# Optimization experiments

Hardware: AMD Instinct MI355X
Metric: run time of the kernel (lower is better)

The kernel has to match this reference:

```python
import math
import jax, jax.numpy as jnp
import numpy as np
from jax.scipy.special import xlogy

B, N, INP, E = 128, 16, 1024, 512
MU, CLF, PLCY = 512, 512, 512
M = N - 1          # merges (full tree)
T = N + M          # total tree tokens
L = N + M - 1      # logits matrix side
NOISE_STD, MASK_VAL = 0.01, -9e20
SFTMX_EPS, STD_EPS = 1e-20, 1e-20


def _mlp3(x, w1, b1, w2, b2, w3, b3):
    h = jax.nn.relu(x @ w1 + b1)
    h = jax.nn.relu(h @ w2 + b2)
    return h @ w3 + b3


def _lin(key, fi, fo):
    lim = math.sqrt(6.0 / (fi + fo))  # xavier uniform
    return (jax.random.uniform(key, (fi, fo), minval=-lim, maxval=lim, dtype=jnp.float32),
            jnp.full((fo,), 0.001, dtype=jnp.float32))


def setup_inputs():
    key = jax.random.key(0)
    ks = jax.random.split(key, 16)
    inp = {"x": jax.random.normal(ks[0], (B, N, INP), dtype=jnp.float32)}
    inp["lift_w"], inp["lift_b"] = _lin(ks[1], INP, E)
    inp["unlift_w"], inp["unlift_b"] = _lin(ks[2], E, INP)
    inp["enc_w1"], inp["enc_b1"] = _lin(ks[3], 2 * E, MU)
    inp["enc_w2"], inp["enc_b2"] = _lin(ks[4], MU, MU)
    inp["enc_w3"], inp["enc_b3"] = _lin(ks[5], MU, E)
    inp["dec_w1"], inp["dec_b1"] = _lin(ks[6], E, MU)
    inp["dec_w2"], inp["dec_b2"] = _lin(ks[7], MU, MU)
    inp["dec_w3"], inp["dec_b3"] = _lin(ks[8], MU, 2 * E)
    inp["clf_w1"], inp["clf_b1"] = _lin(ks[9], E, CLF)
    inp["clf_w2"], inp["clf_b2"] = _lin(ks[10], CLF, CLF)
    inp["clf_w3"], inp["clf_b3"] = _lin(ks[11], CLF, 2)
    inp["pol_w1"], inp["pol_b1"] = _lin(ks[12], 2 * E, PLCY)
    inp["pol_w2"], inp["pol_b2"] = _lin(ks[13], PLCY, PLCY)
    inp["pol_w3"], inp["pol_b3"] = _lin(ks[14], PLCY, 1)
    return inp


def _forward(x, lift_w, lift_b, unlift_w, unlift_b,
             enc_w1, enc_b1, enc_w2, enc_b2, enc_w3, enc_b3,
             dec_w1, dec_b1, dec_w2, dec_b2, dec_w3, dec_b3,
             clf_w1, clf_b1, clf_w2, clf_b2, clf_w3, clf_b3,
             pol_w1, pol_b1, pol_w2, pol_b2, pol_w3, pol_b3):
    sg = jax.lax.stop_gradient
    enc = lambda z: _mlp3(z, enc_w1, enc_b1, enc_w2, enc_b2, enc_w3, enc_b3)
    dec = lambda z: _mlp3(z, dec_w1, dec_b1, dec_w2, dec_b2, dec_w3, dec_b3)
    clf = lambda z: _mlp3(z, clf_w1, clf_b1, clf_w2, clf_b2, clf_w3, clf_b3)
    pol = lambda z: _mlp3(z, pol_w1, pol_b1, pol_w2, pol_b2, pol_w3, pol_b3)
    base = jax.random.key(42)
    b_idx = jnp.arange(B)

    # lift + noise
    u = x @ lift_w + lift_b
    u = u + NOISE_STD * jax.random.normal(jax.random.fold_in(base, 7), u.shape, u.dtype)

    logits_mtx = jnp.full((B, L, L), MASK_VAL, dtype=jnp.float32)
    # iter 0: score all ordered pairs (i,j), i != j, among input tokens (vectorized)
    ii, jj = np.where(~np.eye(N, dtype=bool))                 # P = N*(N-1) static pairs
    pair_x = jnp.concatenate([u[:, ii], u[:, jj]], axis=-1)   # [B,P,2E]
    logits_mtx = logits_mtx.at[:, ii, jj].set(pol(sg(pair_x))[..., 0])

    active = jnp.tile(jnp.arange(N, dtype=jnp.int32), (B, 1))
    step_losses = jnp.zeros(B, dtype=jnp.float32)
    entropies = jnp.zeros(B, dtype=jnp.float32)
    actions, log_probs, rewards = [], [], []

    for it in range(M):
        A = active.shape[1]  # = N - it (active-token count at entry)
        if it > 0:
            nt = N + it - 1                      # newest merged token (last in active)
            act = active[:, :-1]                 # [B, A-1] older active tokens
            u_act = u[b_idx[:, None], act]       # [B, A-1, E]
            u_nt = jnp.broadcast_to(u[:, nt][:, None, :], u_act.shape)
            lg_f = pol(sg(jnp.concatenate([u_nt, u_act], -1)))[..., 0]
            lg_b = pol(sg(jnp.concatenate([u_act, u_nt], -1)))[..., 0]
            logits_mtx = logits_mtx.at[b_idx[:, None], nt, act].set(lg_f)
            logits_mtx = logits_mtx.at[b_idx[:, None], act, nt].set(lg_b)

        flat = logits_mtx.reshape(B, L * L)      # temp == 1 for learned policy
        p = jax.nn.softmax(flat, axis=1)
        P2 = L * L
        p_adj = (p + SFTMX_EPS) / (1.0 + P2 * SFTMX_EPS)
        val_norm = SFTMX_EPS / (1.0 + P2 * SFTMX_EPS)
        opt_norm = A * (A - 1)
        nopt = P2 - opt_norm
        entrop = -(jnp.sum(xlogy(p_adj, p_adj), axis=1)
                   - nopt * (val_norm * math.log(val_norm))) / math.log(opt_norm)
        entropies = entropies + entrop

        # multinomial sample over flattened (masked) logits matrix
        sflat = jax.random.categorical(jax.random.fold_in(base, 100 + it), flat)
        s0, s1 = sflat // L, sflat % L
        sample = jnp.stack([s0, s1], axis=1)     # [B,2]
        actions.append(sample)
        log_probs.append(jnp.log(p[b_idx, sflat]))

        # mask out rows/cols of the merged tokens
        logits_mtx = logits_mtx.at[b_idx[:, None], sample, :].set(MASK_VAL)
        logits_mtx = logits_mtx.at[b_idx[:, None], :, sample].set(MASK_VAL)

        # remove the two sampled tokens from the active set (order-preserving)
        keep = (active != s0[:, None].astype(active.dtype)) & (active != s1[:, None].astype(active.dtype))
        order = jnp.argsort((~keep).astype(jnp.int32), axis=1, stable=True)
        active = jnp.take_along_axis(active, order[:, :A - 2], axis=1)

        pair = jnp.concatenate([u[b_idx, s0], u[b_idx, s1]], axis=1)  # [B,2E]
        true_s = sg(pair)
        pred_s = dec(enc(true_s))
        osl = jnp.sum((pred_s - true_s) ** 2, axis=1) / (2 * E)
        step_losses = step_losses + osl
        rewards.append(-sg(osl))

        # merge: encode pair (grad flows into u here) + noise, append to tree
        mg = enc(pair)
        mg = mg + NOISE_STD * jax.random.normal(jax.random.fold_in(base, 1000 + it), mg.shape, mg.dtype)
        u = jnp.concatenate([u, mg[:, None, :]], axis=1)
        active = jnp.concatenate([active, jnp.full((B, 1), N + it, dtype=active.dtype)], axis=1)

    actions = jnp.stack(actions, axis=1)    # [B,M,2]
    log_probs = jnp.stack(log_probs, axis=1)
    rewards = jnp.stack(rewards, axis=1)

    # top-down decode
    d = jnp.zeros_like(u)
    d = d.at[b_idx[:, None], active].set(u[b_idx[:, None], active])  # seed remaining active (root)
    clf_rows = []
    for it in range(M):
        tok = T - 1 - it
        mgd = d[:, tok]
        unmg = dec(mgd).reshape(B, 2, E)
        d = d.at[b_idx[:, None], actions[:, M - 1 - it]].set(unmg)
        clf_rows.append(clf(sg(mgd)))
    clf_pred = jnp.concatenate(
        [jnp.stack(clf_rows, axis=1), clf(sg(d[:, :N]))[:, ::-1, :]], axis=1)  # [B,M+N,2]
    clf_lbl = jnp.tile(jnp.concatenate(
        [jnp.ones(M, dtype=jnp.int32), jnp.zeros(N, dtype=jnp.int32)]), (B, 1))

    step_losses = step_losses / M
    entropies = entropies / M
    mvg = rewards.reshape(-1)  # B*M <= mvg_adv_sz, so moving buffer == current rewards
    rew_n = (rewards - mvg.mean()) / (jnp.std(mvg, ddof=1) + STD_EPS)
    reinf = jnp.sum(log_probs * rew_n, axis=1)
    recon = d[:, :N] @ unlift_w + unlift_b
    return recon, u, d, step_losses, entropies, clf_pred, clf_lbl, reinf


def reference(x, lift_w, lift_b, unlift_w, unlift_b,
              enc_w1, enc_b1, enc_w2, enc_b2, enc_w3, enc_b3,
              dec_w1, dec_b1, dec_w2, dec_b2, dec_w3, dec_b3,
              clf_w1, clf_b1, clf_w2, clf_b2, clf_w3, clf_b3,
              pol_w1, pol_b1, pol_w2, pol_b2, pol_w3, pol_b3):
    return _forward(x, lift_w, lift_b, unlift_w, unlift_b,
                    enc_w1, enc_b1, enc_w2, enc_b2, enc_w3, enc_b3,
                    dec_w1, dec_b1, dec_w2, dec_b2, dec_w3, dec_b3,
                    clf_w1, clf_b1, clf_w2, clf_b2, clf_w3, clf_b3,
                    pol_w1, pol_b1, pol_w2, pol_b2, pol_w3, pol_b3)
```

## Files before the change

kernel.cpp:

```cpp
#include <hip/hip_runtime.h>
#include <cstdint>
#include <cmath>

#define MASKV -9.0e20f

__host__ __device__ inline void tf2x32(uint32_t k0, uint32_t k1, uint32_t& x0, uint32_t& x1){
  uint32_t ks2 = k0 ^ k1 ^ 0x1BD11BDAu;
  x0 += k0; x1 += k1;
#define TFR(r) { x0 += x1; x1 = (x1<<(r))|(x1>>(32-(r))); x1 ^= x0; }
  TFR(13) TFR(15) TFR(26) TFR(6)
  x0 += k1;  x1 += ks2 + 1u;
  TFR(17) TFR(29) TFR(16) TFR(24)
  x0 += ks2; x1 += k0 + 2u;
  TFR(13) TFR(15) TFR(26) TFR(6)
  x0 += k0;  x1 += k1 + 3u;
  TFR(17) TFR(29) TFR(16) TFR(24)
  x0 += k1;  x1 += ks2 + 4u;
  TFR(13) TFR(15) TFR(26) TFR(6)
  x0 += ks2; x1 += k0 + 5u;
#undef TFR
}

__device__ inline uint32_t rbits32(uint32_t k0, uint32_t k1, uint32_t idx){
  uint32_t x0 = 0u, x1 = idx;
  tf2x32(k0, k1, x0, x1);
  return x0 ^ x1;
}

__device__ inline float u01_from_bits(uint32_t bits){
  union { uint32_t u; float f; } c;
  c.u = (bits >> 9) | 0x3f800000u;
  return c.f - 1.0f;
}

__device__ inline float erfinv_f(float x){
  float w = -log1pf(-x*x);
  float p;
  if (w < 5.0f){
    w -= 2.5f;
    p = 2.81022636e-08f;
    p = fmaf(p, w, 3.43273939e-07f);
    p = fmaf(p, w, -3.5233877e-06f);
    p = fmaf(p, w, -4.39150654e-06f);
    p = fmaf(p, w, 0.00021858087f);
    p = fmaf(p, w, -0.00125372503f);
    p = fmaf(p, w, -0.00417768164f);
    p = fmaf(p, w, 0.246640727f);
    p = fmaf(p, w, 1.50140941f);
  } else {
    w = sqrtf(w) - 3.0f;
    p = -0.000200214257f;
    p = fmaf(p, w, 0.000100950558f);
    p = fmaf(p, w, 0.00134934322f);
    p = fmaf(p, w, -0.00367342844f);
    p = fmaf(p, w, 0.00573950773f);
    p = fmaf(p, w, -0.0076224613f);
    p = fmaf(p, w, 0.00943887047f);
    p = fmaf(p, w, 1.00167406f);
    p = fmaf(p, w, 2.83297682f);
  }
  return p * x;
}

__device__ inline float jax_normal(uint32_t k0, uint32_t k1, uint32_t idx){
  float f = u01_from_bits(rbits32(k0, k1, idx));
  float v = fmaf(f, 2.0f, -0.99999994f);
  v = fmaxf(v, -0.99999994f);
  return 1.41421356f * erfinv_f(v);
}

__device__ inline float jax_gumbel(uint32_t k0, uint32_t k1, uint32_t idx){
  float f = u01_from_bits(rbits32(k0, k1, idx));
  f = f + 1.17549435e-38f;
  f = fmaxf(f, 1.17549435e-38f);
  return -logf(-logf(f));
}

template<int ACT>
__global__ __launch_bounds__(256) void gemm_k(
    const float* __restrict__ A, int lda,
    const long* __restrict__ atab, int anblk,
    const float* __restrict__ W, const float* __restrict__ bias,
    float* __restrict__ C, int K, int N,
    long c_base, int c_rdiv, long c_ostride, long c_istride)
{
  __shared__ float As[16][64];
  __shared__ float Ws[16][64];
  int tid = threadIdx.x;
  int c0 = blockIdx.x * 64;
  int r0 = blockIdx.y * 64;
  int lr = tid >> 2;
  int lk = (tid & 3) << 2;
  int wk = tid >> 4;
  int wc = (tid & 15) << 2;
  int tx = tid & 15;
  int ty = tid >> 4;
  long aoff0 = 0, aoff1 = 0;
  if (atab){
    const long* t = atab + (long)(r0 + lr) * anblk;
    aoff0 = t[0];
    if (anblk == 2) aoff1 = t[1];
  } else {
    aoff0 = (long)(r0 + lr) * lda;
  }
  float acc[4][4];
#pragma unroll
  for (int i = 0; i < 4; i++)
#pragma unroll
    for (int j = 0; j < 4; j++) acc[i][j] = 0.f;

  for (int k0 = 0; k0 < K; k0 += 16){
    int ka = k0 + lk;
    long ab = (atab && anblk == 2 && ka >= 512) ? (aoff1 + (ka - 512)) : (aoff0 + ka);
    float4 av = *(const float4*)(A + ab);
    As[lk + 0][lr] = av.x;
    As[lk + 1][lr] = av.y;
    As[lk + 2][lr] = av.z;
    As[lk + 3][lr] = av.w;
    float4 wv = *(const float4*)(W + (long)(k0 + wk) * N + (c0 + wc));
    *(float4*)&Ws[wk][wc] = wv;
    __syncthreads();
#pragma unroll
    for (int kk = 0; kk < 16; kk++){
      float4 a4 = *(const float4*)&As[kk][ty << 2];
      float4 w4 = *(const float4*)&Ws[kk][tx << 2];
      float aa[4] = {a4.x, a4.y, a4.z, a4.w};
      float ww[4] = {w4.x, w4.y, w4.z, w4.w};
#pragma unroll
      for (int i = 0; i < 4; i++)
#pragma unroll
        for (int j = 0; j < 4; j++)
          acc[i][j] = fmaf(aa[i], ww[j], acc[i][j]);
    }
    __syncthreads();
  }
  float4 bv = *(const float4*)(bias + c0 + (tx << 2));
  float bb[4] = {bv.x, bv.y, bv.z, bv.w};
#pragma unroll
  for (int i = 0; i < 4; i++){
    int r = r0 + (ty << 2) + i;
    long off = c_base + (long)(r / c_rdiv) * c_ostride + (long)(r % c_rdiv) * c_istride
               + c0 + (tx << 2);
    float4 v;
    float o0 = acc[i][0] + bb[0], o1 = acc[i][1] + bb[1];
    float o2 = acc[i][2] + bb[2], o3 = acc[i][3] + bb[3];
    if (ACT){ o0 = fmaxf(o0, 0.f); o1 = fmaxf(o1, 0.f); o2 = fmaxf(o2, 0.f); o3 = fmaxf(o3, 0.f); }
    v.x = o0; v.y = o1; v.z = o2; v.w = o3;
    *(float4*)(C + off) = v;
  }
}

__global__ __launch_bounds__(256) void gemm128f_k(
    const float* __restrict__ Y,
    const long* __restrict__ atab,
    const float* __restrict__ b1,
    const float* __restrict__ W2, const float* __restrict__ b2,
    const float* __restrict__ w3,
    const int* __restrict__ scat, float* __restrict__ logits)
{
  __shared__ float As[16][132];
  __shared__ float Ws[16][132];
  int tid = threadIdx.x;
  int c0 = blockIdx.x * 128;
  int r0 = blockIdx.y * 128;
  int tx = tid & 15, ty = tid >> 4;
  int rA0 = tid >> 2;
  int rA1 = rA0 + 64;
  int kq = (tid & 3) << 2;
  long a00 = atab[(long)(r0 + rA0) * 2];
  long a01 = atab[(long)(r0 + rA0) * 2 + 1];
  long a10 = atab[(long)(r0 + rA1) * 2];
  long a11 = atab[(long)(r0 + rA1) * 2 + 1];
  int wk0 = tid >> 5, wc0 = (tid & 31) << 2;
  float acc[8][8];
#pragma unroll
  for (int i = 0; i < 8; i++)
#pragma unroll
    for (int j = 0; j < 8; j++) acc[i][j] = 0.f;

  for (int k0 = 0; k0 < 512; k0 += 16){
    int ka = k0 + kq;
    float4 p0 = *(const float4*)(Y + a00 + ka);
    float4 q0 = *(const float4*)(Y + a01 + ka);
    float4 p1 = *(const float4*)(Y + a10 + ka);
    float4 q1 = *(const float4*)(Y + a11 + ka);
    float4 bb = *(const float4*)(b1 + ka);
    As[kq + 0][rA0] = fmaxf(p0.x + q0.x + bb.x, 0.f);
    As[kq + 1][rA0] = fmaxf(p0.y + q0.y + bb.y, 0.f);
    As[kq + 2][rA0] = fmaxf(p0.z + q0.z + bb.z, 0.f);
    As[kq + 3][rA0] = fmaxf(p0.w + q0.w + bb.w, 0.f);
    As[kq + 0][rA1] = fmaxf(p1.x + q1.x + bb.x, 0.f);
    As[kq + 1][rA1] = fmaxf(p1.y + q1.y + bb.y, 0.f);
    As[kq + 2][rA1] = fmaxf(p1.z + q1.z + bb.z, 0.f);
    As[kq + 3][rA1] = fmaxf(p1.w + q1.w + bb.w, 0.f);
    *(float4*)&Ws[wk0][wc0]     = *(const float4*)(W2 + (long)(k0 + wk0) * 512 + (c0 + wc0));
    *(float4*)&Ws[wk0 + 8][wc0] = *(const float4*)(W2 + (long)(k0 + wk0 + 8) * 512 + (c0 + wc0));
    __syncthreads();
#pragma unroll
    for (int kk = 0; kk < 16; kk++){
      float a0[8], w0[8];
      *(float4*)&a0[0] = *(const float4*)&As[kk][ty << 2];
      *(float4*)&a0[4] = *(const float4*)&As[kk][(ty << 2) + 64];
      *(float4*)&w0[0] = *(const float4*)&Ws[kk][tx << 2];
      *(float4*)&w0[4] = *(const float4*)&Ws[kk][(tx << 2) + 64];
#pragma unroll
      for (int i = 0; i < 8; i++)
#pragma unroll
        for (int j = 0; j < 8; j++)
          acc[i][j] = fmaf(a0[i], w0[j], acc[i][j]);
    }
    __syncthreads();
  }
  float bb[8], w3v[8];
  *(float4*)&bb[0]  = *(const float4*)(b2 + c0 + (tx << 2));
  *(float4*)&bb[4]  = *(const float4*)(b2 + c0 + (tx << 2) + 64);
  *(float4*)&w3v[0] = *(const float4*)(w3 + c0 + (tx << 2));
  *(float4*)&w3v[4] = *(const float4*)(w3 + c0 + (tx << 2) + 64);
#pragma unroll
  for (int i = 0; i < 8; i++){
    float p = 0.f;
#pragma unroll
    for (int j = 0; j < 8; j++)
      p = fmaf(fmaxf(acc[i][j] + bb[j], 0.f), w3v[j], p);
    for (int m = 1; m < 16; m <<= 1) p += __shfl_xor(p, m);
    if (tx == 0){
      int rr = (i < 4) ? ((ty << 2) + i) : (64 + (ty << 2) + (i - 4));
      atomicAdd(logits + scat[r0 + rr], p);
    }
  }
}

__global__ __launch_bounds__(256) void gemm64f_k(
    const float* __restrict__ Y,
    const long* __restrict__ atab,
    const float* __restrict__ b1,
    const float* __restrict__ W2, const float* __restrict__ b2,
    const float* __restrict__ w3,
    const int* __restrict__ scat, float* __restrict__ logits)
{
  __shared__ float As[16][64];
  __shared__ float Ws[16][64];
  int tid = threadIdx.x;
  int c0 = blockIdx.x * 64;
  int r0 = blockIdx.y * 64;
  int lr = tid >> 2;
  int lk = (tid & 3) << 2;
  int wk = tid >> 4;
  int wc = (tid & 15) << 2;
  int tx = tid & 15;
  int ty = tid >> 4;
  long a0 = atab[(long)(r0 + lr) * 2];
  long a1 = atab[(long)(r0 + lr) * 2 + 1];
  float acc[4][4];
#pragma unroll
  for (int i = 0; i < 4; i++)
#pragma unroll
    for (int j = 0; j < 4; j++) acc[i][j] = 0.f;

  for (int k0 = 0; k0 < 512; k0 += 16){
    int ka = k0 + lk;
    float4 p = *(const float4*)(Y + a0 + ka);
    float4 q = *(const float4*)(Y + a1 + ka);
    float4 bb = *(const float4*)(b1 + ka);
    As[lk + 0][lr] = fmaxf(p.x + q.x + bb.x, 0.f);
    As[lk + 1][lr] = fmaxf(p.y + q.y + bb.y, 0.f);
    As[lk + 2][lr] = fmaxf(p.z + q.z + bb.z, 0.f);
    As[lk + 3][lr] = fmaxf(p.w + q.w + bb.w, 0.f);
    *(float4*)&Ws[wk][wc] = *(const float4*)(W2 + (long)(k0 + wk) * 512 + (c0 + wc));
    __syncthreads();
#pragma unroll
    for (int kk = 0; kk < 16; kk++){
      float4 a4 = *(const float4*)&As[kk][ty << 2];
      float4 w4 = *(const float4*)&Ws[kk][tx << 2];
      float aa[4] = {a4.x, a4.y, a4.z, a4.w};
      float ww[4] = {w4.x, w4.y, w4.z, w4.w};
#pragma unroll
      for (int i = 0; i < 4; i++)
#pragma unroll
        for (int j = 0; j < 4; j++)
          acc[i][j] = fmaf(aa[i], ww[j], acc[i][j]);
    }
    __syncthreads();
  }
  float bb4[4], w34[4];
  *(float4*)&bb4[0] = *(const float4*)(b2 + c0 + (tx << 2));
  *(float4*)&w34[0] = *(const float4*)(w3 + c0 + (tx << 2));
#pragma unroll
  for (int i = 0; i < 4; i++){
    float p = 0.f;
#pragma unroll
    for (int j = 0; j < 4; j++)
      p = fmaf(fmaxf(acc[i][j] + bb4[j], 0.f), w34[j], p);
    for (int m = 1; m < 16; m <<= 1) p += __shfl_xor(p, m);
    if (tx == 0){
      int r = r0 + (ty << 2) + i;
      atomicAdd(logits + scat[r], p);
    }
  }
}

__global__ __launch_bounds__(256) void rowdot2_k(
    const float* __restrict__ A, int lda,
    const float* __restrict__ W, const float* __restrict__ bias,
    int K, float* __restrict__ out, const int* __restrict__ scat)
{
  int wid = threadIdx.x >> 6, lane = threadIdx.x & 63;
  int r = blockIdx.x * 4 + wid;
  const float* a = A + (long)r * lda;
  float s0 = 0.f, s1 = 0.f;
  for (int k = lane; k < K; k += 64){
    float x = a[k];
    s0 = fmaf(x, W[k * 2], s0);
    s1 = fmaf(x, W[k * 2 + 1], s1);
  }
  for (int off = 32; off > 0; off >>= 1){
    s0 += __shfl_down(s0, off);
    s1 += __shfl_down(s1, off);
  }
  if (lane == 0){
    long o = scat[r];
    out[o] = s0 + bias[0];
    out[o + 1] = s1 + bias[1];
  }
}

__global__ __launch_bounds__(256) void pairmv_k(
    const float* __restrict__ u, const long* __restrict__ tab_pair,
    const float* __restrict__ W, const float* __restrict__ bias,
    float* __restrict__ dst)
{
  __shared__ float s[1024];
  int b = blockIdx.y, tid = threadIdx.x;
  int c = blockIdx.x * 256 + tid;
  long t0 = tab_pair[b * 2], t1 = tab_pair[b * 2 + 1];
  s[tid]       = u[t0 + tid];
  s[tid + 256] = u[t0 + tid + 256];
  s[tid + 512] = u[t1 + tid];
  s[tid + 768] = u[t1 + tid + 256];
  __syncthreads();
  float a0 = 0.f, a1 = 0.f, a2 = 0.f, a3 = 0.f;
#pragma unroll 8
  for (int k = 0; k < 1024; k += 4){
    a0 = fmaf(s[k],     W[(long)k * 512 + c],       a0);
    a1 = fmaf(s[k + 1], W[(long)(k + 1) * 512 + c], a1);
    a2 = fmaf(s[k + 2], W[(long)(k + 2) * 512 + c], a2);
    a3 = fmaf(s[k + 3], W[(long)(k + 3) * 512 + c], a3);
  }
  float v = ((a0 + a1) + (a2 + a3)) + bias[c];
  dst[(long)b * 512 + c] = fmaxf(v, 0.f);
}

__global__ __launch_bounds__(256) void mvrelu_k(
    const float* __restrict__ src, long sstride,
    const float* __restrict__ W, const float* __restrict__ bias,
    float* __restrict__ dst)
{
  __shared__ float s[512];
  int b = blockIdx.y, tid = threadIdx.x;
  int c = blockIdx.x * 256 + tid;
  const float* sr = src + (long)b * sstride;
  s[tid] = sr[tid];
  s[tid + 256] = sr[tid + 256];
  __syncthreads();
  float a0 = 0.f, a1 = 0.f, a2 = 0.f, a3 = 0.f;
#pragma unroll 8
// ... 101 lines not shown
    float d0 = p[k] - t0[k];       s = fmaf(d0, d0, s);
    float d1 = p[k + 512] - t1[k]; s = fmaf(d1, d1, s);
  }
  __shared__ float red[256];
  red[tid] = s; __syncthreads();
  for (int st = 128; st > 0; st >>= 1){ if (tid < st) red[tid] += red[tid + st]; __syncthreads(); }
  if (tid == 0){
    float osl = red[0] / 1024.0f;
    atomicAdd(sl + b, osl);
    rew[b * 15 + it] = -osl;
  }
}

__global__ __launch_bounds__(256) void init_k(float* __restrict__ lbl,
    float* __restrict__ logits, float* __restrict__ sl, float* __restrict__ ent,
    int* __restrict__ active, float* __restrict__ zb,
    float* __restrict__ W1cat, const float* __restrict__ pol_w1, const float* __restrict__ pol_b3,
    long* __restrict__ tab_init, int* __restrict__ scat_init, long* __restrict__ tab_tok16,
    long* __restrict__ tab_mgd, int* __restrict__ scat_clf, long clf_off)
{
  long i = (long)blockIdx.x * 256 + threadIdx.x;
  if (i < 524288L){
    int k = (int)(i >> 10), n = (int)(i & 1023);
    W1cat[i] = (n < 512) ? pol_w1[(long)k * 512 + n] : pol_w1[(long)(k + 512) * 512 + (n - 512)];
  }
  if (i < 115200L){
    int rem = (int)(i % 900);
    int rr = rem / 30, cc = rem % 30;
    logits[i] = (rr < 16 && cc < 16 && rr != cc) ? pol_b3[0] : MASKV;
  }
  if (i < 30720L){
    int r = (int)i;
    int pk = r >> 7, b = r & 127;
    int ii2 = pk / 15, jr = pk % 15;
    int jj2 = jr + (jr >= ii2 ? 1 : 0);
    tab_init[r * 2]     = ((long)(b * 31 + ii2)) * 1024;
    tab_init[r * 2 + 1] = ((long)(b * 31 + jj2)) * 1024 + 512;
    scat_init[r] = b * 900 + ii2 * 30 + jj2;
  }
  if (i < 3968L){
    lbl[i] = ((i % 31) < 15) ? 1.0f : 0.0f;
    int r = (int)i;
    if (r < 1920){
      scat_clf[r] = (int)(clf_off + (long)(r & 127) * 62 + (r >> 7) * 2);
    } else {
      int rr = r - 1920;
      scat_clf[r] = (int)(clf_off + (long)(rr >> 4) * 62 + 60 - ((rr & 15) << 1));
    }
  }
  if (i < 2048L){
    active[i] = (int)(i & 15);
    tab_tok16[i] = ((long)((i >> 4) * 31 + (i & 15))) * 512;
  }
  if (i < 1920L){
    int it = (int)(i >> 7), b = (int)(i & 127);
    tab_mgd[i] = ((long)(b * 31 + 30 - it)) * 512;
  }
  if (i < 1024L)  zb[i] = 0.f;
  if (i < 128L){ sl[i] = 0.f; ent[i] = 0.f; }
}

__global__ __launch_bounds__(256) void noise_u_k(float* __restrict__ u, uint32_t k0, uint32_t k1){
  uint32_t e = blockIdx.x * 256u + threadIdx.x;
  uint32_t b = e >> 13, rem = e & 8191u, n = rem >> 9, ee = rem & 511u;
  float nr = jax_normal(k0, k1, e);
  long off = ((long)(b * 31u + n)) * 512 + ee;
  u[off] += 0.01f * nr;
}

__global__ __launch_bounds__(256) void build_d_k(float* __restrict__ dmat, const float* __restrict__ u){
  int e = blockIdx.x * 256 + threadIdx.x;
  int b = e >> 9, ee = e & 511;
  long off = ((long)(b * 31 + 30)) * 512 + ee;
  dmat[off] = u[off];
}

__global__ __launch_bounds__(256) void sample_k(float* __restrict__ logits, int* __restrict__ active,
    int* __restrict__ actions, float* __restrict__ lp, float* __restrict__ ent,
    int it, int A, uint32_t k0, uint32_t k1, float log_opt,
    long* __restrict__ tab_loop, int* __restrict__ scat_loop, long* __restrict__ tab_pair,
    const float* __restrict__ pol_b3)
{
  int b = blockIdx.x, tid = threadIdx.x;
  float* Lg = logits + (long)b * 900;
  __shared__ float red[256];
  __shared__ int redi[256];
  __shared__ int ss0, ss1;

  float v = -3.4e38f;
  for (int j = tid; j < 900; j += 256) v = fmaxf(v, Lg[j]);
  red[tid] = v; __syncthreads();
  for (int s = 128; s > 0; s >>= 1){ if (tid < s) red[tid] = fmaxf(red[tid], red[tid + s]); __syncthreads(); }
  float m = red[0]; __syncthreads();

  float acc = 0.f;
  for (int j = tid; j < 900; j += 256) acc += expf(Lg[j] - m);
  red[tid] = acc; __syncthreads();
  for (int s = 128; s > 0; s >>= 1){ if (tid < s) red[tid] += red[tid + s]; __syncthreads(); }
  float ssum = red[0]; __syncthreads();

  float es = 0.f;
  for (int j = tid; j < 900; j += 256){
    float l = Lg[j];
    if (l > MASKV){
      float p = expf(l - m) / ssum;
      float pa = p + 1e-20f;
      es += pa * logf(pa);
    }
  }
  red[tid] = es; __syncthreads();
  for (int s = 128; s > 0; s >>= 1){ if (tid < s) red[tid] += red[tid + s]; __syncthreads(); }
  if (tid == 0) ent[b] += -(red[0]) / log_opt;
  __syncthreads();

  float bv = -3.4e38f; int bi = 0;
  for (int j = tid; j < 900; j += 256){
    float g = jax_gumbel(k0, k1, (uint32_t)(b * 900 + j));
    float val = Lg[j] + g;
    if (val > bv){ bv = val; bi = j; }
  }
  red[tid] = bv; redi[tid] = bi; __syncthreads();
  for (int s = 128; s > 0; s >>= 1){
    if (tid < s){
      float o = red[tid + s]; int oi = redi[tid + s];
      if (o > red[tid] || (o == red[tid] && oi < redi[tid])){ red[tid] = o; redi[tid] = oi; }
    }
    __syncthreads();
  }
  if (tid == 0){
    int sf = redi[0];
    int s0 = sf / 30, s1 = sf % 30;
    ss0 = s0; ss1 = s1;
    actions[(b * 15 + it) * 2] = s0;
    actions[(b * 15 + it) * 2 + 1] = s1;
    lp[b * 15 + it] = Lg[sf] - m - logf(ssum);
    tab_pair[b * 2]     = ((long)(b * 31 + s0)) * 512;
    tab_pair[b * 2 + 1] = ((long)(b * 31 + s1)) * 512;
  }
  __syncthreads();
  int s0 = ss0, s1 = ss1;
  if (tid < 30){
    Lg[s0 * 30 + tid] = MASKV;
    Lg[s1 * 30 + tid] = MASKV;
    Lg[tid * 30 + s0] = MASKV;
    Lg[tid * 30 + s1] = MASKV;
  }
  if (tid == 0){
    float b3v = pol_b3[0];
    int buf[16]; int c = 0;
    for (int k = 0; k < A; k++){
      int a = active[b * 16 + k];
      if (a != s0 && a != s1) buf[c++] = a;
    }
    int nt2 = 16 + it;
    buf[c++] = nt2;
    for (int k = 0; k < c; k++) active[b * 16 + k] = buf[k];
    int na2 = c - 1;
    for (int j = 0; j < na2; j++){
      int q = buf[j];
      int r1 = j * 128 + b;
      tab_loop[r1 * 2]     = ((long)(b * 31 + nt2)) * 1024;
      tab_loop[r1 * 2 + 1] = ((long)(b * 31 + q)) * 1024 + 512;
      int sc1 = b * 900 + nt2 * 30 + q;
      scat_loop[r1] = sc1;
      logits[sc1] = b3v;
      int r2 = (na2 + j) * 128 + b;
      tab_loop[r2 * 2]     = ((long)(b * 31 + q)) * 1024;
      tab_loop[r2 * 2 + 1] = ((long)(b * 31 + nt2)) * 1024 + 512;
      int sc2 = b * 900 + q * 30 + nt2;
      scat_loop[r2] = sc2;
      logits[sc2] = b3v;
    }
  }
}

__global__ __launch_bounds__(256) void finalize_k(const float* __restrict__ rew,
    const float* __restrict__ lp, const float* __restrict__ sl, const float* __restrict__ ent,
    float* __restrict__ out_sl, float* __restrict__ out_ent, float* __restrict__ out_reinf)
{
  __shared__ float red[256];
  int tid = threadIdx.x;
  float s = 0.f;
  for (int i = tid; i < 1920; i += 256) s += rew[i];
  red[tid] = s; __syncthreads();
  for (int st = 128; st > 0; st >>= 1){ if (tid < st) red[tid] += red[tid + st]; __syncthreads(); }
  float mean = red[0] / 1920.0f; __syncthreads();
  float v = 0.f;
  for (int i = tid; i < 1920; i += 256){ float x = rew[i] - mean; v = fmaf(x, x, v); }
  red[tid] = v; __syncthreads();
  for (int st = 128; st > 0; st >>= 1){ if (tid < st) red[tid] += red[tid + st]; __syncthreads(); }
  float denom = sqrtf(red[0] / 1919.0f) + 1e-20f;
  if (tid < 128){
    out_sl[tid] = sl[tid] / 15.0f;
    out_ent[tid] = ent[tid] / 15.0f;
    float r = 0.f;
    for (int k = 0; k < 15; k++){
      float rn = (rew[tid * 15 + k] - mean) / denom;
      r = fmaf(lp[tid * 15 + k], rn, r);
    }
    out_reinf[tid] = r;
  }
}

extern "C" void kernel_launch(void* const* d_in, const int* in_sizes, int n_in,
                              void* d_out, int out_size, void* d_ws, size_t ws_size,
                              hipStream_t stream)
{
  const float* x        = (const float*)d_in[0];
  const float* lift_w   = (const float*)d_in[1];
  const float* lift_b   = (const float*)d_in[2];
  const float* unlift_w = (const float*)d_in[3];
  const float* unlift_b = (const float*)d_in[4];
  const float* enc_w1   = (const float*)d_in[5];
  const float* enc_b1   = (const float*)d_in[6];
  const float* enc_w2   = (const float*)d_in[7];
  const float* enc_b2   = (const float*)d_in[8];
  const float* enc_w3   = (const float*)d_in[9];
  const float* enc_b3   = (const float*)d_in[10];
// ... 7 lines not shown
  const float* clf_b1   = (const float*)d_in[18];
  const float* clf_w2   = (const float*)d_in[19];
  const float* clf_b2   = (const float*)d_in[20];
  const float* clf_w3   = (const float*)d_in[21];
  const float* clf_b3   = (const float*)d_in[22];
  const float* pol_w1   = (const float*)d_in[23];
  const float* pol_b1   = (const float*)d_in[24];
  const float* pol_w2   = (const float*)d_in[25];
  const float* pol_b2   = (const float*)d_in[26];
  const float* pol_w3   = (const float*)d_in[27];
  const float* pol_b3   = (const float*)d_in[28];

  float* out = (float*)d_out;
  const long U_OFF     = 2097152;
  const long D_OFF     = 4128768;
  const long SL_OFF    = 6160384;
  const long ENT_OFF   = 6160512;
  const long CLF_OFF   = 6160640;
  const long LBL_OFF   = 6168576;
  const long REINF_OFF = 6172544;
  float* recon = out;
  float* u     = out + U_OFF;
  float* dmat  = out + D_OFF;

  char* wsb = (char*)d_ws;
  size_t wo = 0;
  auto alloc = [&](size_t bytes) -> void* {
    void* p = (void*)(wsb + wo);
    wo = (wo + bytes + 255) & ~(size_t)255;
    return p;
  };
  float* logits    = (float*)alloc(115200 * 4);
  float* Y         = (float*)alloc((size_t)3968 * 1024 * 4);
  float* h1clf     = Y;
  float* pbuf      = Y + 2031616;
  float* h2clf     = Y + 2031616;
  float* W1cat     = (float*)alloc((size_t)524288 * 4);
  float* zb        = (float*)alloc(1024 * 4);
  float* h1        = (float*)alloc((size_t)2048 * 512 * 4);
  float* h2        = (float*)alloc((size_t)2048 * 512 * 4);
  float* z_all     = (float*)alloc((size_t)15 * 65536 * 4);
  float* sl        = (float*)alloc(128 * 4);
  float* ent       = (float*)alloc(128 * 4);
  float* lp        = (float*)alloc(1920 * 4);
  float* rew       = (float*)alloc(1920 * 4);
  int*   active    = (int*)alloc(2048 * 4);
  int*   actions   = (int*)alloc(3840 * 4);
  long*  tab_init  = (long*)alloc((size_t)30720 * 2 * 8);
  int*   scat_init = (int*)alloc(30720 * 4);
  long*  tab_loop  = (long*)alloc((size_t)3584 * 2 * 8);
  int*   scat_loop = (int*)alloc(3584 * 4);
  long*  tab_pair  = (long*)alloc(256 * 8);
  long*  tab_mgd   = (long*)alloc(1920 * 8);
  long*  tab_tok16 = (long*)alloc(2048 * 8);
  int*   scat_clf  = (int*)alloc(3968 * 4);
  long*  tab_clf   = tab_mgd;
  (void)ws_size; (void)in_sizes; (void)n_in; (void)out_size;

  uint32_t k7a, k7b, ck0[15], ck1[15], mk0[15], mk1[15];
  { uint32_t a = 0, b = 7; tf2x32(0u, 42u, a, b); k7a = a; k7b = b; }
  for (int it = 0; it < 15; it++){
    { uint32_t a = 0, b = (uint32_t)(100 + it); tf2x32(0u, 42u, a, b); ck0[it] = a; ck1[it] = b; }
    { uint32_t a = 0, b = (uint32_t)(1000 + it); tf2x32(0u, 42u, a, b); mk0[it] = a; mk1[it] = b; }
  }

  auto gemm = [&](int act, const float* A, int lda, const long* atab, int anblk,
                  const float* W, const float* bs, float* C, int rows, int K, int Nn,
                  long cb, int crd, long cos, long cis){
    dim3 g(Nn / 64, rows / 64);
    if (act) gemm_k<1><<<g, 256, 0, stream>>>(A, lda, atab, anblk, W, bs, C, K, Nn, cb, crd, cos, cis);
    else     gemm_k<0><<<g, 256, 0, stream>>>(A, lda, atab, anblk, W, bs, C, K, Nn, cb, crd, cos, cis);
  };

  init_k<<<2048, 256, 0, stream>>>(out + LBL_OFF, logits, sl, ent, active, zb,
                                   W1cat, pol_w1, pol_b3, tab_init, scat_init, tab_tok16,
                                   tab_mgd, scat_clf, CLF_OFF);

  gemm(0, x, 1024, nullptr, 0, lift_w, lift_b, u, 2048, 1024, 512, 0, 16, 15872, 512);
  noise_u_k<<<4096, 256, 0, stream>>>(u, k7a, k7b);

  gemm(0, u, 0, tab_tok16, 1, W1cat, zb, Y, 2048, 512, 1024, 0, 16, 31744, 1024);

  { dim3 g(4, 240);
    gemm128f_k<<<g, 256, 0, stream>>>(Y, tab_init, pol_b1, pol_w2, pol_b2, pol_w3,
                                      scat_init, logits); }

  for (int it = 0; it < 15; it++){
    int A = 16 - it;
    if (it > 0){
      int rows = 256 * (15 - it);
      dim3 g(8, rows / 64);
      gemm64f_k<<<g, 256, 0, stream>>>(Y, tab_loop, pol_b1, pol_w2, pol_b2, pol_w3,
                                       scat_loop, logits);
    }
    float log_opt = (float)log((double)(A * (A - 1)));
    sample_k<<<128, 256, 0, stream>>>(logits, active, actions, lp, ent, it, A,
                                      ck0[it], ck1[it], log_opt,
                                      tab_loop, scat_loop, tab_pair, pol_b3);
    { dim3 g(2, 128);
      pairmv_k<<<g, 256, 0, stream>>>(u, tab_pair, enc_w1, enc_b1, h1); }
    { dim3 g(2, 128);
      mvrelu_k<<<g, 256, 0, stream>>>(h1, 512, enc_w2, enc_b2, h2); }
    { dim3 g(2, 128);
      lay3z_k<<<g, 256, 0, stream>>>(h2, enc_w3, enc_b3, z_all, u, it, mk0[it], mk1[it]); }
    if (it < 14){
      dim3 g(4, 128);
      yrow_k<<<g, 256, 0, stream>>>(u, W1cat, Y, it);
    }
  }

  gemm(1, z_all, 512, nullptr, 0, dec_w1, dec_b1, h1, 1920, 512, 512, 0, 1, 512, 0);
  gemm(1, h1, 512, nullptr, 0, dec_w2, dec_b2, h2, 1920, 512, 512, 0, 1, 512, 0);
  gemm(0, h2, 512, nullptr, 0, dec_w3, dec_b3, pbuf, 1920, 512, 1024, 0, 1, 1024, 0);
  oslb_k<<<1920, 256, 0, stream>>>(pbuf, u, actions, sl, rew);

  build_d_k<<<256, 256, 0, stream>>>(dmat, u);

  for (int it = 0; it < 15; it++){
    int tok = 30 - it;
    { dim3 g(2, 128);
      mvrelu_k<<<g, 256, 0, stream>>>(dmat + (long)tok * 512, 15872, dec_w1, dec_b1, h1); }
    { dim3 g(2, 128);
      mvrelu_k<<<g, 256, 0, stream>>>(h1, 512, dec_w2, dec_b2, h2); }
    { dim3 g(4, 128);
      rev3_k<<<g, 256, 0, stream>>>(h2, dec_w3, dec_b3, dmat, actions, it); }
  }

  gemm(1, dmat, 0, tab_clf, 1, clf_w1, clf_b1, h1clf, 3968, 512, 512, 0, 1, 512, 0);
  gemm(1, h1clf, 512, nullptr, 0, clf_w2, clf_b2, h2clf, 3968, 512, 512, 0, 1, 512, 0);
  rowdot2_k<<<992, 256, 0, stream>>>(h2clf, 512, clf_w3, clf_b3, 512, out, scat_clf);

  gemm(0, dmat, 0, tab_tok16, 1, unlift_w, unlift_b, recon, 2048, 512, 1024,
       0, 16, 16384, 1024);

  finalize_k<<<1, 256, 0, stream>>>(rew, lp, sl, ent,
                                    out + SL_OFF, out + ENT_OFF, out + REINF_OFF);
}
```

Measured before the change: 2.578 ms.

## Double-buffer shared tiles in GEMM kernels and use wave-shuffle reductions in sampling

The three SGEMM kernels now keep two shared-memory tile buffers and prefetch the next K-slice into registers while computing on the current one, so each iteration needs one barrier instead of two and global load latency overlaps the FMAs. The sampling kernel replaces tree reductions in shared memory with 64-lane shuffle reductions plus a small cross-wave step. It also computes entropy algebraically from a single pass (sum of e*d over S, minus log S), removing a reduction pass. The changes cost more shared memory and registers, which may lower occupancy, and the algebraic entropy can differ slightly in floating-point rounding from the original.

```diff
diff --git a/kernel.cpp b/kernel.cpp
--- a/kernel.cpp
+++ b/kernel.cpp
@@ -84,8 +84,8 @@
     float* __restrict__ C, int K, int N,
     long c_base, int c_rdiv, long c_ostride, long c_istride)
 {
-  __shared__ float As[16][64];
-  __shared__ float Ws[16][64];
+  __shared__ float As[2][16][64];
+  __shared__ float Ws[2][16][64];
   int tid = threadIdx.x;
   int c0 = blockIdx.x * 64;
   int r0 = blockIdx.y * 64;
@@ -109,21 +109,30 @@
 #pragma unroll
     for (int j = 0; j < 4; j++) acc[i][j] = 0.f;
 
+  {
+    float4 av = *(const float4*)(A + aoff0 + lk);
+    As[0][lk + 0][lr] = av.x;
+    As[0][lk + 1][lr] = av.y;
+    As[0][lk + 2][lr] = av.z;
+    As[0][lk + 3][lr] = av.w;
+    *(float4*)&Ws[0][wk][wc] = *(const float4*)(W + (long)wk * N + (c0 + wc));
+  }
+  __syncthreads();
+
+  int pb = 0;
   for (int k0 = 0; k0 < K; k0 += 16){
-    int ka = k0 + lk;
-    long ab = (atab && anblk == 2 && ka >= 512) ? (aoff1 + (ka - 512)) : (aoff0 + ka);
-    float4 av = *(const float4*)(A + ab);
-    As[lk + 0][lr] = av.x;
-    As[lk + 1][lr] = av.y;
-    As[lk + 2][lr] = av.z;
-    As[lk + 3][lr] = av.w;
-    float4 wv = *(const float4*)(W + (long)(k0 + wk) * N + (c0 + wc));
-    *(float4*)&Ws[wk][wc] = wv;
-    __syncthreads();
+    int nk = k0 + 16;
+    float4 av, wv;
+    if (nk < K){
+      int ka = nk + lk;
+      long ab = (atab && anblk == 2 && ka >= 512) ? (aoff1 + (ka - 512)) : (aoff0 + ka);
+      av = *(const float4*)(A + ab);
+      wv = *(const float4*)(W + (long)(nk + wk) * N + (c0 + wc));
+    }
 #pragma unroll
     for (int kk = 0; kk < 16; kk++){
-      float4 a4 = *(const float4*)&As[kk][ty << 2];
-      float4 w4 = *(const float4*)&Ws[kk][tx << 2];
+      float4 a4 = *(const float4*)&As[pb][kk][ty << 2];
+      float4 w4 = *(const float4*)&Ws[pb][kk][tx << 2];
       float aa[4] = {a4.x, a4.y, a4.z, a4.w};
       float ww[4] = {w4.x, w4.y, w4.z, w4.w};
 #pragma unroll
@@ -132,7 +141,16 @@
         for (int j = 0; j < 4; j++)
           acc[i][j] = fmaf(aa[i], ww[j], acc[i][j]);
     }
+    if (nk < K){
+      int nb = pb ^ 1;
+      As[nb][lk + 0][lr] = av.x;
+      As[nb][lk + 1][lr] = av.y;
+      As[nb][lk + 2][lr] = av.z;
+      As[nb][lk + 3][lr] = av.w;
+      *(float4*)&Ws[nb][wk][wc] = wv;
+    }
     __syncthreads();
+    pb ^= 1;
   }
   float4 bv = *(const float4*)(bias + c0 + (tx << 2));
   float bb[4] = {bv.x, bv.y, bv.z, bv.w};
@@ -158,8 +176,8 @@
     const float* __restrict__ w3,
     const int* __restrict__ scat, float* __restrict__ logits)
 {
-  __shared__ float As[16][132];
-  __shared__ float Ws[16][132];
+  __shared__ float As[2][16][132];
+  __shared__ float Ws[2][16][132];
   int tid = threadIdx.x;
   int c0 = blockIdx.x * 128;
   int r0 = blockIdx.y * 128;
@@ -178,38 +196,67 @@
 #pragma unroll
     for (int j = 0; j < 8; j++) acc[i][j] = 0.f;
 
+  {
+    float4 p0 = *(const float4*)(Y + a00 + kq);
+    float4 q0 = *(const float4*)(Y + a01 + kq);
+    float4 p1 = *(const float4*)(Y + a10 + kq);
+    float4 q1 = *(const float4*)(Y + a11 + kq);
+    float4 bb = *(const float4*)(b1 + kq);
+    As[0][kq + 0][rA0] = fmaxf(p0.x + q0.x + bb.x, 0.f);
+    As[0][kq + 1][rA0] = fmaxf(p0.y + q0.y + bb.y, 0.f);
+    As[0][kq + 2][rA0] = fmaxf(p0.z + q0.z + bb.z, 0.f);
+    As[0][kq + 3][rA0] = fmaxf(p0.w + q0.w + bb.w, 0.f);
+    As[0][kq + 0][rA1] = fmaxf(p1.x + q1.x + bb.x, 0.f);
+    As[0][kq + 1][rA1] = fmaxf(p1.y + q1.y + bb.y, 0.f);
+    As[0][kq + 2][rA1] = fmaxf(p1.z + q1.z + bb.z, 0.f);
+    As[0][kq + 3][rA1] = fmaxf(p1.w + q1.w + bb.w, 0.f);
+    *(float4*)&Ws[0][wk0][wc0]     = *(const float4*)(W2 + (long)wk0 * 512 + (c0 + wc0));
+    *(float4*)&Ws[0][wk0 + 8][wc0] = *(const float4*)(W2 + (long)(wk0 + 8) * 512 + (c0 + wc0));
+  }
+  __syncthreads();
+
+  int pb = 0;
   for (int k0 = 0; k0 < 512; k0 += 16){
-    int ka = k0 + kq;
-    float4 p0 = *(const float4*)(Y + a00 + ka);
-    float4 q0 = *(const float4*)(Y + a01 + ka);
-    float4 p1 = *(const float4*)(Y + a10 + ka);
-    float4 q1 = *(const float4*)(Y + a11 + ka);
-    float4 bb = *(const float4*)(b1 + ka);
-    As[kq + 0][rA0] = fmaxf(p0.x + q0.x + bb.x, 0.f);
-    As[kq + 1][rA0] = fmaxf(p0.y + q0.y + bb.y, 0.f);
-    As[kq + 2][rA0] = fmaxf(p0.z + q0.z + bb.z, 0.f);
-    As[kq + 3][rA0] = fmaxf(p0.w + q0.w + bb.w, 0.f);
-    As[kq + 0][rA1] = fmaxf(p1.x + q1.x + bb.x, 0.f);
-    As[kq + 1][rA1] = fmaxf(p1.y + q1.y + bb.y, 0.f);
-    As[kq + 2][rA1] = fmaxf(p1.z + q1.z + bb.z, 0.f);
-    As[kq + 3][rA1] = fmaxf(p1.w + q1.w + bb.w, 0.f);
-    *(float4*)&Ws[wk0][wc0]     = *(const float4*)(W2 + (long)(k0 + wk0) * 512 + (c0 + wc0));
-    *(float4*)&Ws[wk0 + 8][wc0] = *(const float4*)(W2 + (long)(k0 + wk0 + 8) * 512 + (c0 + wc0));
-    __syncthreads();
+    int nk = k0 + 16;
+    float4 p0, q0, p1, q1, bb, w0v, w1v;
+    if (nk < 512){
+      int ka = nk + kq;
+      p0 = *(const float4*)(Y + a00 + ka);
+      q0 = *(const float4*)(Y + a01 + ka);
+      p1 = *(const float4*)(Y + a10 + ka);
+      q1 = *(const float4*)(Y + a11 + ka);
+      bb = *(const float4*)(b1 + ka);
+      w0v = *(const float4*)(W2 + (long)(nk + wk0) * 512 + (c0 + wc0));
+      w1v = *(const float4*)(W2 + (long)(nk + wk0 + 8) * 512 + (c0 + wc0));
+    }
 #pragma unroll
     for (int kk = 0; kk < 16; kk++){
       float a0[8], w0[8];
-      *(float4*)&a0[0] = *(const float4*)&As[kk][ty << 2];
-      *(float4*)&a0[4] = *(const float4*)&As[kk][(ty << 2) + 64];
-      *(float4*)&w0[0] = *(const float4*)&Ws[kk][tx << 2];
-      *(float4*)&w0[4] = *(const float4*)&Ws[kk][(tx << 2) + 64];
+      *(float4*)&a0[0] = *(const float4*)&As[pb][kk][ty << 2];
+      *(float4*)&a0[4] = *(const float4*)&As[pb][kk][(ty << 2) + 64];
+      *(float4*)&w0[0] = *(const float4*)&Ws[pb][kk][tx << 2];
+      *(float4*)&w0[4] = *(const float4*)&Ws[pb][kk][(tx << 2) + 64];
 #pragma unroll
       for (int i = 0; i < 8; i++)
 #pragma unroll
         for (int j = 0; j < 8; j++)
           acc[i][j] = fmaf(a0[i], w0[j], acc[i][j]);
     }
+    if (nk < 512){
+      int nb = pb ^ 1;
+      As[nb][kq + 0][rA0] = fmaxf(p0.x + q0.x + bb.x, 0.f);
+      As[nb][kq + 1][rA0] = fmaxf(p0.y + q0.y + bb.y, 0.f);
+      As[nb][kq + 2][rA0] = fmaxf(p0.z + q0.z + bb.z, 0.f);
+      As[nb][kq + 3][rA0] = fmaxf(p0.w + q0.w + bb.w, 0.f);
+      As[nb][kq + 0][rA1] = fmaxf(p1.x + q1.x + bb.x, 0.f);
+      As[nb][kq + 1][rA1] = fmaxf(p1.y + q1.y + bb.y, 0.f);
+      As[nb][kq + 2][rA1] = fmaxf(p1.z + q1.z + bb.z, 0.f);
+      As[nb][kq + 3][rA1] = fmaxf(p1.w + q1.w + bb.w, 0.f);
+      *(float4*)&Ws[nb][wk0][wc0]     = w0v;
+      *(float4*)&Ws[nb][wk0 + 8][wc0] = w1v;
+    }
     __syncthreads();
+    pb ^= 1;
   }
   float bb[8], w3v[8];
   *(float4*)&bb[0]  = *(const float4*)(b2 + c0 + (tx << 2));
@@ -238,8 +285,8 @@
     const float* __restrict__ w3,
     const int* __restrict__ scat, float* __restrict__ logits)
 {
-  __shared__ float As[16][64];
-  __shared__ float Ws[16][64];
+  __shared__ float As[2][16][64];
+  __shared__ float Ws[2][16][64];
   int tid = threadIdx.x;
   int c0 = blockIdx.x * 64;
   int r0 = blockIdx.y * 64;
@@ -257,21 +304,33 @@
 #pragma unroll
     for (int j = 0; j < 4; j++) acc[i][j] = 0.f;
 
+  {
+    float4 p = *(const float4*)(Y + a0 + lk);
+    float4 q = *(const float4*)(Y + a1 + lk);
+    float4 bb = *(const float4*)(b1 + lk);
+    As[0][lk + 0][lr] = fmaxf(p.x + q.x + bb.x, 0.f);
+    As[0][lk + 1][lr] = fmaxf(p.y + q.y + bb.y, 0.f);
+    As[0][lk + 2][lr] = fmaxf(p.z + q.z + bb.z, 0.f);
+    As[0][lk + 3][lr] = fmaxf(p.w + q.w + bb.w, 0.f);
+    *(float4*)&Ws[0][wk][wc] = *(const float4*)(W2 + (long)wk * 512 + (c0 + wc));
+  }
+  __syncthreads();
+
+  int pb = 0;
   for (int k0 = 0; k0 < 512; k0 += 16){
-    int ka = k0 + lk;
-    float4 p = *(const float4*)(Y + a0 + ka);
-    float4 q = *(const float4*)(Y + a1 + ka);
-    float4 bb = *(const float4*)(b1 + ka);
-    As[lk + 0][lr] = fmaxf(p.x + q.x + bb.x, 0.f);
-    As[lk + 1][lr] = fmaxf(p.y + q.y + bb.y, 0.f);
-    As[lk + 2][lr] = fmaxf(p.z + q.z + bb.z, 0.f);
-    As[lk + 3][lr] = fmaxf(p.w + q.w + bb.w, 0.f);
-    *(float4*)&Ws[wk][wc] = *(const float4*)(W2 + (long)(k0 + wk) * 512 + (c0 + wc));
-    __syncthreads();
+    int nk = k0 + 16;
+    float4 p, q, bb, wv;
+    if (nk < 512){
+      int ka = nk + lk;
+      p = *(const float4*)(Y + a0 + ka);
+      q = *(const float4*)(Y + a1 + ka);
+      bb = *(const float4*)(b1 + ka);
+      wv = *(const float4*)(W2 + (long)(nk + wk) * 512 + (c0 + wc));
+    }
 #pragma unroll
     for (int kk = 0; kk < 16; kk++){
-      float4 a4 = *(const float4*)&As[kk][ty << 2];
-      float4 w4 = *(const float4*)&Ws[kk][tx << 2];
+      float4 a4 = *(const float4*)&As[pb][kk][ty << 2];
+      float4 w4 = *(const float4*)&Ws[pb][kk][tx << 2];
       float aa[4] = {a4.x, a4.y, a4.z, a4.w};
       float ww[4] = {w4.x, w4.y, w4.z, w4.w};
 #pragma unroll
@@ -280,7 +339,16 @@
         for (int j = 0; j < 4; j++)
           acc[i][j] = fmaf(aa[i], ww[j], acc[i][j]);
     }
+    if (nk < 512){
+      int nb = pb ^ 1;
+      As[nb][lk + 0][lr] = fmaxf(p.x + q.x + bb.x, 0.f);
+      As[nb][lk + 1][lr] = fmaxf(p.y + q.y + bb.y, 0.f);
+      As[nb][lk + 2][lr] = fmaxf(p.z + q.z + bb.z, 0.f);
+      As[nb][lk + 3][lr] = fmaxf(p.w + q.w + bb.w, 0.f);
+      *(float4*)&Ws[nb][wk][wc] = wv;
+    }
     __syncthreads();
+    pb ^= 1;
   }
   float bb4[4], w34[4];
   *(float4*)&bb4[0] = *(const float4*)(b2 + c0 + (tx << 2));
@@ -548,36 +616,32 @@
     const float* __restrict__ pol_b3)
 {
   int b = blockIdx.x, tid = threadIdx.x;
+  int lane = tid & 63, wid = tid >> 6;
   float* Lg = logits + (long)b * 900;
-  __shared__ float red[256];
-  __shared__ int redi[256];
+  __shared__ float rmax[4], rS[4], rT[4], rG[4];
+  __shared__ int rGi[4];
+  __shared__ float smx, sS;
   __shared__ int ss0, ss1;
 
   float v = -3.4e38f;
   for (int j = tid; j < 900; j += 256) v = fmaxf(v, Lg[j]);
-  red[tid] = v; __syncthreads();
-  for (int s = 128; s > 0; s >>= 1){ if (tid < s) red[tid] = fmaxf(red[tid], red[tid + s]); __syncthreads(); }
-  float m = red[0]; __syncthreads();
-
-  float acc = 0.f;
-  for (int j = tid; j < 900; j += 256) acc += expf(Lg[j] - m);
-  red[tid] = acc; __syncthreads();
-  for (int s = 128; s > 0; s >>= 1){ if (tid < s) red[tid] += red[tid + s]; __syncthreads(); }
-  float ssum = red[0]; __syncthreads();
-
-  float es = 0.f;
+#pragma unroll
+  for (int m = 32; m; m >>= 1) v = fmaxf(v, __shfl_xor(v, m));
+  if (lane == 0) rmax[wid] = v;
+  __syncthreads();
+  float mx = fmaxf(fmaxf(rmax[0], rmax[1]), fmaxf(rmax[2], rmax[3]));
+
+  float s = 0.f, t = 0.f;
   for (int j = tid; j < 900; j += 256){
     float l = Lg[j];
-    if (l > MASKV){
-      float p = expf(l - m) / ssum;
-      float pa = p + 1e-20f;
-      es += pa * logf(pa);
-    }
-  }
-  red[tid] = es; __syncthreads();
-  for (int s = 128; s > 0; s >>= 1){ if (tid < s) red[tid] += red[tid + s]; __syncthreads(); }
-  if (tid == 0) ent[b] += -(red[0]) / log_opt;
-  __syncthreads();
+    float d = l - mx;
+    float e = expf(d);
+    s += e;
+    if (l > MASKV) t = fmaf(e, d, t);
+  }
+#pragma unroll
+  for (int m = 32; m; m >>= 1){ s += __shfl_xor(s, m); t += __shfl_xor(t, m); }
+  if (lane == 0){ rS[wid] = s; rT[wid] = t; }
 
   float bv = -3.4e38f; int bi = 0;
   for (int j = tid; j < 900; j += 256){
@@ -585,21 +649,29 @@
     float val = Lg[j] + g;
     if (val > bv){ bv = val; bi = j; }
   }
-  red[tid] = bv; redi[tid] = bi; __syncthreads();
-  for (int s = 128; s > 0; s >>= 1){
-    if (tid < s){
-      float o = red[tid + s]; int oi = redi[tid + s];
-      if (o > red[tid] || (o == red[tid] && oi < redi[tid])){ red[tid] = o; redi[tid] = oi; }
-    }
-    __syncthreads();
-  }
+#pragma unroll
+  for (int m = 32; m; m >>= 1){
+    float ov = __shfl_xor(bv, m); int oi = __shfl_xor(bi, m);
+    if (ov > bv || (ov == bv && oi < bi)){ bv = ov; bi = oi; }
+  }
+  if (lane == 0){ rG[wid] = bv; rGi[wid] = bi; }
+  __syncthreads();
+
   if (tid == 0){
-    int sf = redi[0];
+    float S = (rS[0] + rS[1]) + (rS[2] + rS[3]);
+    float T = (rT[0] + rT[1]) + (rT[2] + rT[3]);
+    ent[b] += -(T / S - logf(S)) / log_opt;
+    float gb = rG[0]; int gi = rGi[0];
+    for (int w = 1; w < 4; w++){
+      if (rG[w] > gb || (rG[w] == gb && rGi[w] < gi)){ gb = rG[w]; gi = rGi[w]; }
+    }
+    int sf = gi;
     int s0 = sf / 30, s1 = sf % 30;
     ss0 = s0; ss1 = s1;
+    smx = mx; sS = S;
     actions[(b * 15 + it) * 2] = s0;
     actions[(b * 15 + it) * 2 + 1] = s1;
-    lp[b * 15 + it] = Lg[sf] - m - logf(ssum);
+    lp[b * 15 + it] = Lg[sf] - mx - logf(S);
     tab_pair[b * 2]     = ((long)(b * 31 + s0)) * 512;
     tab_pair[b * 2 + 1] = ((long)(b * 31 + s1)) * 512;
   }
```

Result: no change. 2.580 ms (+0.1%).

## Retile initial policy GEMM to 512 threads and fuse sample reductions with shuffles

Applied to the files above, without the earlier changes.

The initial fused policy GEMM now runs 512 threads per block, each computing a 4x8 output tile instead of 8x8. This halves per-thread registers and loads, aiming for better occupancy. The sampling kernel swaps its shared-memory tree reductions for wave-level shuffle reductions. It also folds the sum-exp and entropy passes into one pass using the identity entropy = log S - T/S, which removes several barriers and a full pass over the logits. The entropy identity drops the 1e-20 epsilon, so results may differ slightly from the reference.

```diff
diff --git a/kernel.cpp b/kernel.cpp
--- a/kernel.cpp
+++ b/kernel.cpp
@@ -150,7 +150,7 @@
   }
 }
 
-__global__ __launch_bounds__(256) void gemm128f_k(
+__global__ __launch_bounds__(512, 7) void gemm128f_k(
     const float* __restrict__ Y,
     const long* __restrict__ atab,
     const float* __restrict__ b1,
@@ -164,50 +164,40 @@
   int c0 = blockIdx.x * 128;
   int r0 = blockIdx.y * 128;
   int tx = tid & 15, ty = tid >> 4;
-  int rA0 = tid >> 2;
-  int rA1 = rA0 + 64;
+  int rA = tid >> 2;
   int kq = (tid & 3) << 2;
-  long a00 = atab[(long)(r0 + rA0) * 2];
-  long a01 = atab[(long)(r0 + rA0) * 2 + 1];
-  long a10 = atab[(long)(r0 + rA1) * 2];
-  long a11 = atab[(long)(r0 + rA1) * 2 + 1];
-  int wk0 = tid >> 5, wc0 = (tid & 31) << 2;
-  float acc[8][8];
-#pragma unroll
-  for (int i = 0; i < 8; i++)
+  long a0r = atab[(long)(r0 + rA) * 2];
+  long a1r = atab[(long)(r0 + rA) * 2 + 1];
+  int wk = tid >> 5;
+  int wc = (tid & 31) << 2;
+  float acc[4][8];
+#pragma unroll
+  for (int i = 0; i < 4; i++)
 #pragma unroll
     for (int j = 0; j < 8; j++) acc[i][j] = 0.f;
 
   for (int k0 = 0; k0 < 512; k0 += 16){
     int ka = k0 + kq;
-    float4 p0 = *(const float4*)(Y + a00 + ka);
-    float4 q0 = *(const float4*)(Y + a01 + ka);
-    float4 p1 = *(const float4*)(Y + a10 + ka);
-    float4 q1 = *(const float4*)(Y + a11 + ka);
+    float4 p = *(const float4*)(Y + a0r + ka);
+    float4 q = *(const float4*)(Y + a1r + ka);
     float4 bb = *(const float4*)(b1 + ka);
-    As[kq + 0][rA0] = fmaxf(p0.x + q0.x + bb.x, 0.f);
-    As[kq + 1][rA0] = fmaxf(p0.y + q0.y + bb.y, 0.f);
-    As[kq + 2][rA0] = fmaxf(p0.z + q0.z + bb.z, 0.f);
-    As[kq + 3][rA0] = fmaxf(p0.w + q0.w + bb.w, 0.f);
-    As[kq + 0][rA1] = fmaxf(p1.x + q1.x + bb.x, 0.f);
-    As[kq + 1][rA1] = fmaxf(p1.y + q1.y + bb.y, 0.f);
-    As[kq + 2][rA1] = fmaxf(p1.z + q1.z + bb.z, 0.f);
-    As[kq + 3][rA1] = fmaxf(p1.w + q1.w + bb.w, 0.f);
-    *(float4*)&Ws[wk0][wc0]     = *(const float4*)(W2 + (long)(k0 + wk0) * 512 + (c0 + wc0));
-    *(float4*)&Ws[wk0 + 8][wc0] = *(const float4*)(W2 + (long)(k0 + wk0 + 8) * 512 + (c0 + wc0));
+    As[kq + 0][rA] = fmaxf(p.x + q.x + bb.x, 0.f);
+    As[kq + 1][rA] = fmaxf(p.y + q.y + bb.y, 0.f);
+    As[kq + 2][rA] = fmaxf(p.z + q.z + bb.z, 0.f);
+    As[kq + 3][rA] = fmaxf(p.w + q.w + bb.w, 0.f);
+    *(float4*)&Ws[wk][wc] = *(const float4*)(W2 + (long)(k0 + wk) * 512 + (c0 + wc));
     __syncthreads();
 #pragma unroll
     for (int kk = 0; kk < 16; kk++){
-      float a0[8], w0[8];
-      *(float4*)&a0[0] = *(const float4*)&As[kk][ty << 2];
-      *(float4*)&a0[4] = *(const float4*)&As[kk][(ty << 2) + 64];
-      *(float4*)&w0[0] = *(const float4*)&Ws[kk][tx << 2];
-      *(float4*)&w0[4] = *(const float4*)&Ws[kk][(tx << 2) + 64];
-#pragma unroll
-      for (int i = 0; i < 8; i++)
+      float a4[4], w8[8];
+      *(float4*)&a4[0] = *(const float4*)&As[kk][ty << 2];
+      *(float4*)&w8[0] = *(const float4*)&Ws[kk][tx << 2];
+      *(float4*)&w8[4] = *(const float4*)&Ws[kk][(tx << 2) + 64];
+#pragma unroll
+      for (int i = 0; i < 4; i++)
 #pragma unroll
         for (int j = 0; j < 8; j++)
-          acc[i][j] = fmaf(a0[i], w0[j], acc[i][j]);
+          acc[i][j] = fmaf(a4[i], w8[j], acc[i][j]);
     }
     __syncthreads();
   }
@@ -217,14 +207,14 @@
   *(float4*)&w3v[0] = *(const float4*)(w3 + c0 + (tx << 2));
   *(float4*)&w3v[4] = *(const float4*)(w3 + c0 + (tx << 2) + 64);
 #pragma unroll
-  for (int i = 0; i < 8; i++){
+  for (int i = 0; i < 4; i++){
     float p = 0.f;
 #pragma unroll
     for (int j = 0; j < 8; j++)
       p = fmaf(fmaxf(acc[i][j] + bb[j], 0.f), w3v[j], p);
     for (int m = 1; m < 16; m <<= 1) p += __shfl_xor(p, m);
     if (tx == 0){
-      int rr = (i < 4) ? ((ty << 2) + i) : (64 + (ty << 2) + (i - 4));
+      int rr = (ty << 2) + i;
       atomicAdd(logits + scat[r0 + rr], p);
     }
   }
@@ -548,36 +538,31 @@
     const float* __restrict__ pol_b3)
 {
   int b = blockIdx.x, tid = threadIdx.x;
+  int lane = tid & 63, wid = tid >> 6;
   float* Lg = logits + (long)b * 900;
-  __shared__ float red[256];
-  __shared__ int redi[256];
+  __shared__ float rmax[4], rS[4], rT[4], rG[4];
+  __shared__ int rGi[4];
   __shared__ int ss0, ss1;
 
   float v = -3.4e38f;
   for (int j = tid; j < 900; j += 256) v = fmaxf(v, Lg[j]);
-  red[tid] = v; __syncthreads();
-  for (int s = 128; s > 0; s >>= 1){ if (tid < s) red[tid] = fmaxf(red[tid], red[tid + s]); __syncthreads(); }
-  float m = red[0]; __syncthreads();
-
-  float acc = 0.f;
-  for (int j = tid; j < 900; j += 256) acc += expf(Lg[j] - m);
-  red[tid] = acc; __syncthreads();
-  for (int s = 128; s > 0; s >>= 1){ if (tid < s) red[tid] += red[tid + s]; __syncthreads(); }
-  float ssum = red[0]; __syncthreads();
-
-  float es = 0.f;
+#pragma unroll
+  for (int m = 32; m; m >>= 1) v = fmaxf(v, __shfl_xor(v, m));
+  if (lane == 0) rmax[wid] = v;
+  __syncthreads();
+  float mx = fmaxf(fmaxf(rmax[0], rmax[1]), fmaxf(rmax[2], rmax[3]));
+
+  float s = 0.f, t = 0.f;
   for (int j = tid; j < 900; j += 256){
     float l = Lg[j];
-    if (l > MASKV){
-      float p = expf(l - m) / ssum;
-      float pa = p + 1e-20f;
-      es += pa * logf(pa);
-    }
-  }
-  red[tid] = es; __syncthreads();
-  for (int s = 128; s > 0; s >>= 1){ if (tid < s) red[tid] += red[tid + s]; __syncthreads(); }
-  if (tid == 0) ent[b] += -(red[0]) / log_opt;
-  __syncthreads();
+    float d = l - mx;
+    float e = expf(d);
+    s += e;
+    if (l > MASKV) t = fmaf(e, d, t);
+  }
+#pragma unroll
+  for (int m = 32; m; m >>= 1){ s += __shfl_xor(s, m); t += __shfl_xor(t, m); }
+  if (lane == 0){ rS[wid] = s; rT[wid] = t; }
 
   float bv = -3.4e38f; int bi = 0;
   for (int j = tid; j < 900; j += 256){
@@ -585,21 +570,28 @@
     float val = Lg[j] + g;
     if (val > bv){ bv = val; bi = j; }
   }
-  red[tid] = bv; redi[tid] = bi; __syncthreads();
-  for (int s = 128; s > 0; s >>= 1){
-    if (tid < s){
-      float o = red[tid + s]; int oi = redi[tid + s];
-      if (o > red[tid] || (o == red[tid] && oi < redi[tid])){ red[tid] = o; redi[tid] = oi; }
-    }
-    __syncthreads();
-  }
+#pragma unroll
+  for (int m = 32; m; m >>= 1){
+    float ov = __shfl_xor(bv, m); int oi = __shfl_xor(bi, m);
+    if (ov > bv || (ov == bv && oi < bi)){ bv = ov; bi = oi; }
+  }
+  if (lane == 0){ rG[wid] = bv; rGi[wid] = bi; }
+  __syncthreads();
+
   if (tid == 0){
-    int sf = redi[0];
+    float S = (rS[0] + rS[1]) + (rS[2] + rS[3]);
+    float T = (rT[0] + rT[1]) + (rT[2] + rT[3]);
+    ent[b] += -(T / S - logf(S)) / log_opt;
+    float gb = rG[0]; int gi = rGi[0];
+    for (int w = 1; w < 4; w++){
+      if (rG[w] > gb || (rG[w] == gb && rGi[w] < gi)){ gb = rG[w]; gi = rGi[w]; }
+    }
+    int sf = gi;
     int s0 = sf / 30, s1 = sf % 30;
     ss0 = s0; ss1 = s1;
     actions[(b * 15 + it) * 2] = s0;
     actions[(b * 15 + it) * 2 + 1] = s1;
-    lp[b * 15 + it] = Lg[sf] - m - logf(ssum);
+    lp[b * 15 + it] = Lg[sf] - mx - logf(S);
     tab_pair[b * 2]     = ((long)(b * 31 + s0)) * 512;
     tab_pair[b * 2 + 1] = ((long)(b * 31 + s1)) * 512;
   }
@@ -773,7 +765,7 @@
   gemm(0, u, 0, tab_tok16, 1, W1cat, zb, Y, 2048, 512, 1024, 0, 16, 31744, 1024);
 
   { dim3 g(4, 240);
-    gemm128f_k<<<g, 256, 0, stream>>>(Y, tab_init, pol_b1, pol_w2, pol_b2, pol_w3,
+    gemm128f_k<<<g, 512, 0, stream>>>(Y, tab_init, pol_b1, pol_w2, pol_b2, pol_w3,
                                       scat_init, logits); }
 
   for (int it = 0; it < 15; it++){
```

Result: no change. 2.568 ms (-0.4%).
